# Performance work log

Measured on AMD Instinct MI355X. Metric: run time of the kernel, lower is better.

## Reference

```python
import math
import jax, jax.numpy as jnp
import numpy as np

NUM_HEADS = 16
D_MODEL = 1024
D_HEAD = 64
D_SEQ = 2048
NUM_LAYERS = 24
BATCH = 2


def setup_inputs() -> dict:
    key = jax.random.key(0)
    ks = jax.random.split(key, 10)
    s = math.sqrt(0.02)
    residual = jax.random.normal(ks[0], (BATCH, D_SEQ, D_MODEL), dtype=jnp.float32)
    W_Q = jax.random.normal(ks[1], (NUM_HEADS, D_MODEL, D_HEAD), dtype=jnp.float32) * s
    W_K = jax.random.normal(ks[2], (NUM_HEADS, D_MODEL, D_HEAD), dtype=jnp.float32) * s
    W_V = jax.random.normal(ks[3], (NUM_HEADS, D_MODEL, D_HEAD), dtype=jnp.float32) * s
    W_O = jax.random.normal(ks[4], (NUM_HEADS * D_HEAD, D_MODEL), dtype=jnp.float32) * s
    W_O = W_O / math.sqrt(NUM_LAYERS)
    b_Q = jax.random.normal(ks[5], (NUM_HEADS, D_HEAD), dtype=jnp.float32) * s
    b_K = jax.random.normal(ks[6], (NUM_HEADS, D_HEAD), dtype=jnp.float32) * s
    b_V = jax.random.normal(ks[7], (NUM_HEADS, D_HEAD), dtype=jnp.float32) * s
    b_O = jax.random.normal(ks[8], (D_MODEL,), dtype=jnp.float32) * s
    return dict(residual=residual, W_Q=W_Q, W_K=W_K, W_V=W_V, W_O=W_O,
                b_Q=b_Q, b_K=b_K, b_V=b_V, b_O=b_O)


def reference(residual, W_Q, W_K, W_V, W_O, b_Q, b_K, b_V, b_O):
    # residual: [b, s, m]; W_{Q,K,V}: [h, m, d]; b_{Q,K,V}: [h, d]
    Q = jnp.einsum('hmd,bsm->bshd', W_Q, residual) + b_Q
    K = jnp.einsum('hmd,bsm->bshd', W_K, residual) + b_K
    V = jnp.einsum('hmd,bsm->bshd', W_V, residual) + b_V
    # full causal score matrix [b, h, s_q, s_k], masked with -inf above diagonal
    QK = jnp.einsum('bqhd,bkhd->bhqk', Q, K)
    seq = residual.shape[1]
    causal = jnp.triu(jnp.ones((seq, seq), dtype=bool), k=1)  # True above diag
    QK_masked = jnp.where(causal, -jnp.inf, QK)
    soft = jax.nn.softmax(QK_masked / math.sqrt(D_HEAD), axis=-1)
    attn = jnp.einsum('bhqk,bkhd->bqhd', soft, V)  # [b, s, h, d]
    multi_head = attn.reshape(attn.shape[0], attn.shape[1], NUM_HEADS * D_HEAD)
    return jnp.einsum('em,bqe->bqm', W_O, multi_head) + b_O
```

## Files before the change

kernel.cpp:

```cpp
#include <hip/hip_runtime.h>
#include <stdint.h>

typedef unsigned short u16;
typedef unsigned long long u64;
typedef _Float16 f16;
typedef __attribute__((ext_vector_type(8))) _Float16 f16x8;
typedef __attribute__((ext_vector_type(4))) float f32x4;
typedef __attribute__((ext_vector_type(16))) float f32x16;
typedef __attribute__((ext_vector_type(4))) unsigned short u16x4;
typedef __attribute__((ext_vector_type(8))) unsigned short u16x8;

#define NHEADS 16
#define DMODEL 1024
#define DHEAD 64
#define SEQ 2048
#define NBATCH 2
#define MROWS (NBATCH * SEQ)
#define NQKV 3072
#define SCQ 0.18033688011112042f

__device__ __forceinline__ u16 f2h(float x) {
  union { f16 h; u16 u; } v;
  v.h = (f16)x;
  return v.u;
}

__device__ __forceinline__ unsigned pk2u(float x, float y) {
  typedef __fp16 fp16x2 __attribute__((ext_vector_type(2)));
  fp16x2 h = __builtin_amdgcn_cvt_pkrtz(x, y);
  union { fp16x2 h; unsigned u; } v; v.h = h;
  return v.u;
}

__device__ __forceinline__ f16x8 mkfrag(unsigned w0, unsigned w1, unsigned w2, unsigned w3) {
  union { unsigned u[4]; f16x8 f; } t;
  t.u[0] = w0; t.u[1] = w1; t.u[2] = w2; t.u[3] = w3;
  return t.f;
}

__device__ __forceinline__ f16x8 vfrag(const char* row, int sz, int F, int hib8) {
  union { u64 u[2]; f16x8 f; } t;
  t.u[0] = *(const u64*)(row + (((2 * F) ^ sz) << 4) + hib8);
  t.u[1] = *(const u64*)(row + (((2 * F + 1) ^ sz) << 4) + hib8);
  return t.f;
}

__device__ __forceinline__ void gload_lds16(const void* g, void* l) {
  __builtin_amdgcn_global_load_lds(
      (const __attribute__((address_space(1))) void*)g,
      (__attribute__((address_space(3))) void*)l, 16, 0, 0);
}

__global__ __launch_bounds__(256) void prep_kernel(
    const float* __restrict__ X,
    const float* __restrict__ WQ, const float* __restrict__ WK,
    const float* __restrict__ WV, const float* __restrict__ WO,
    u16* __restrict__ Xh, u16* __restrict__ Wqkv, u16* __restrict__ Wo) {
  __shared__ u16 lt[64][72];
  int blk = blockIdx.x;
  if (blk < 2048) {
    int i = blk * 256 + threadIdx.x;
    const f32x4* xv = (const f32x4*)(X + (size_t)i * 8);
    f32x4 a = xv[0], b = xv[1];
    u16x8 o;
    o[0] = f2h(a[0]); o[1] = f2h(a[1]); o[2] = f2h(a[2]); o[3] = f2h(a[3]);
    o[4] = f2h(b[0]); o[5] = f2h(b[1]); o[6] = f2h(b[2]); o[7] = f2h(b[3]);
    *(u16x8*)(Xh + (size_t)i * 8) = o;
  } else if (blk < 2816) {
    int bb = blk - 2048;
    int mt = bb & 15, hh = (bb >> 4) & 15, qkv = bb >> 8;
    const float* W = (qkv == 0) ? WQ : (qkv == 1) ? WK : WV;
    int m_in = threadIdx.x >> 2, dq = threadIdx.x & 3;
    const f32x4* sp4 = (const f32x4*)(W + (size_t)hh * (DMODEL * DHEAD) +
                                      (size_t)(mt * 64 + m_in) * DHEAD + dq * 16);
#pragma unroll
    for (int v4 = 0; v4 < 4; ++v4) {
      f32x4 a = sp4[v4];
#pragma unroll
      for (int j = 0; j < 4; ++j) lt[dq * 16 + v4 * 4 + j][m_in] = f2h(a[j]);
    }
    __syncthreads();
    int d_in = threadIdx.x >> 2, mq = threadIdx.x & 3;
    size_t orow = ((size_t)(qkv * 1024 + hh * 64 + d_in)) * DMODEL + mt * 64 + mq * 16;
    u16x8 o0, o1;
#pragma unroll
    for (int j = 0; j < 8; ++j) {
      o0[j] = lt[d_in][mq * 16 + j];
      o1[j] = lt[d_in][mq * 16 + 8 + j];
    }
    *(u16x8*)(Wqkv + orow) = o0;
    *(u16x8*)(Wqkv + orow + 8) = o1;
  } else {
    int bb = blk - 2816;
    int mt = bb & 15, et = bb >> 4;
    int e_in = threadIdx.x >> 2, mq = threadIdx.x & 3;
    const f32x4* sp4 = (const f32x4*)(WO + (size_t)(et * 64 + e_in) * DMODEL + mt * 64 + mq * 16);
#pragma unroll
    for (int v4 = 0; v4 < 4; ++v4) {
      f32x4 a = sp4[v4];
#pragma unroll
      for (int j = 0; j < 4; ++j) lt[mq * 16 + v4 * 4 + j][e_in] = f2h(a[j]);
    }
    __syncthreads();
    int m_in = threadIdx.x >> 2, eq = threadIdx.x & 3;
    size_t orow = (size_t)(mt * 64 + m_in) * DMODEL + et * 64 + eq * 16;
    u16x8 o0, o1;
#pragma unroll
    for (int j = 0; j < 8; ++j) {
      o0[j] = lt[m_in][eq * 16 + j];
      o1[j] = lt[m_in][eq * 16 + 8 + j];
    }
    *(u16x8*)(Wo + orow) = o0;
    *(u16x8*)(Wo + orow + 8) = o1;
  }
}

__global__ __launch_bounds__(256, 2) void gemm_qkv(
    const u16* __restrict__ A, const u16* __restrict__ Bt,
    const float* __restrict__ bq, const float* __restrict__ bk, const float* __restrict__ bv,
    u16* __restrict__ Qo, u16* __restrict__ Ko, u16* __restrict__ Vto) {
  __shared__ u16 lds[2][8192];
  const int tid = threadIdx.x;
  const int wid = tid >> 6, lane = tid & 63, lr = lane & 15, lg = lane >> 4;
  const int wr = wid >> 1, wc = wid & 1;
  const int brow = blockIdx.y * 128, bcol = blockIdx.x * 128;

  f32x4 acc[4][4];
#pragma unroll
  for (int i = 0; i < 4; ++i)
#pragma unroll
    for (int j = 0; j < 4; ++j) acc[i][j] = (f32x4){0.f, 0.f, 0.f, 0.f};

#define STAGE(buf, kt)                                                               \
  {                                                                                  \
    _Pragma("unroll") for (int i = 0; i < 2; ++i) {                                  \
      int idx = tid + i * 256;                                                       \
      gload_lds16(A + (size_t)(brow + (idx >> 2)) * 1024 + (kt) * 32 + (idx & 3) * 8,\
                  (char*)&lds[buf][0] + (wid * 64 + i * 256) * 16);                  \
    }                                                                                \
    _Pragma("unroll") for (int i = 0; i < 2; ++i) {                                  \
      int idx = tid + i * 256;                                                       \
      gload_lds16(Bt + (size_t)(bcol + (idx >> 2)) * 1024 + (kt) * 32 + (idx & 3) * 8,\
                  (char*)&lds[buf][4096] + (wid * 64 + i * 256) * 16);               \
    }                                                                                \
  }

  STAGE(0, 0);
  __syncthreads();
  int cur = 0;
  for (int kt = 0; kt < 32; ++kt) {
    if (kt + 1 < 32) STAGE(cur ^ 1, kt + 1);
    const u16* Ab = &lds[cur][0];
    const u16* Bb = &lds[cur][4096];
    f16x8 a[4], b[4];
#pragma unroll
    for (int ar = 0; ar < 4; ++ar)
      a[ar] = *(const f16x8*)(Ab + (wr * 64 + ar * 16 + lr) * 32 + lg * 8);
#pragma unroll
    for (int bc = 0; bc < 4; ++bc)
      b[bc] = *(const f16x8*)(Bb + (wc * 64 + bc * 16 + lr) * 32 + lg * 8);
#pragma unroll
    for (int ar = 0; ar < 4; ++ar)
#pragma unroll
      for (int bc = 0; bc < 4; ++bc)
        acc[ar][bc] = __builtin_amdgcn_mfma_f32_16x16x32_f16(a[ar], b[bc], acc[ar][bc], 0, 0, 0);
    __syncthreads();
    cur ^= 1;
  }

#pragma unroll
  for (int ar = 0; ar < 4; ++ar) {
    int row0 = brow + wr * 64 + ar * 16 + lg * 4;
    int bb = row0 >> 11, s0 = row0 & 2047;
#pragma unroll
    for (int bc = 0; bc < 4; ++bc) {
      int n = bcol + wc * 64 + bc * 16 + lr;
      int qkv = n >> 10, hd = n & 1023, h = hd >> 6, d = hd & 63;
      float bias = ((qkv == 0) ? bq : (qkv == 1) ? bk : bv)[hd];
      if (qkv < 2) {
        u16* dst = qkv ? Ko : Qo;
        float sc = qkv ? 1.f : SCQ;
        size_t base = ((size_t)(bb * NHEADS + h) * SEQ + s0) * DHEAD + d;
#pragma unroll
        for (int r = 0; r < 4; ++r)
          dst[base + (size_t)r * DHEAD] = f2h((acc[ar][bc][r] + bias) * sc);
      } else {
        u16x4 o;
        o[0] = f2h(acc[ar][bc][0] + bias);
        o[1] = f2h(acc[ar][bc][1] + bias);
        o[2] = f2h(acc[ar][bc][2] + bias);
        o[3] = f2h(acc[ar][bc][3] + bias);
        *(u16x4*)(Vto + ((size_t)(bb * NHEADS + h) * DHEAD + d) * SEQ + s0) = o;
      }
    }
  }
}

__global__ __launch_bounds__(256, 2) void gemm_out(
    const u16* __restrict__ A, const u16* __restrict__ Bt,
    const float* __restrict__ bo, float* __restrict__ Co) {
  __shared__ u16 lds[2][8192];
  const int tid = threadIdx.x;
  const int wid = tid >> 6, lane = tid & 63, lr = lane & 15, lg = lane >> 4;
  const int wr = wid >> 1, wc = wid & 1;
  const int brow = blockIdx.y * 128, bcol = blockIdx.x * 128;

  f32x4 acc[4][4];
#pragma unroll
  for (int i = 0; i < 4; ++i)
#pragma unroll
    for (int j = 0; j < 4; ++j) acc[i][j] = (f32x4){0.f, 0.f, 0.f, 0.f};

  STAGE(0, 0);
  __syncthreads();
  int cur = 0;
  for (int kt = 0; kt < 32; ++kt) {
    if (kt + 1 < 32) STAGE(cur ^ 1, kt + 1);
    const u16* Ab = &lds[cur][0];
    const u16* Bb = &lds[cur][4096];
    f16x8 a[4], b[4];
#pragma unroll
    for (int ar = 0; ar < 4; ++ar)
      a[ar] = *(const f16x8*)(Ab + (wr * 64 + ar * 16 + lr) * 32 + lg * 8);
#pragma unroll
    for (int bc = 0; bc < 4; ++bc)
      b[bc] = *(const f16x8*)(Bb + (wc * 64 + bc * 16 + lr) * 32 + lg * 8);
#pragma unroll
    for (int ar = 0; ar < 4; ++ar)
#pragma unroll
      for (int bc = 0; bc < 4; ++bc)
        acc[ar][bc] = __builtin_amdgcn_mfma_f32_16x16x32_f16(a[ar], b[bc], acc[ar][bc], 0, 0, 0);
    __syncthreads();
    cur ^= 1;
  }
#undef STAGE

#pragma unroll
  for (int ar = 0; ar < 4; ++ar) {
    int row0 = brow + wr * 64 + ar * 16 + lg * 4;
#pragma unroll
    for (int bc = 0; bc < 4; ++bc) {
      int n = bcol + wc * 64 + bc * 16 + lr;
      float bias = bo[n];
#pragma unroll
      for (int r = 0; r < 4; ++r)
        Co[(size_t)(row0 + r) * DMODEL + n] = acc[ar][bc][r] + bias;
    }
  }
}

__global__ __launch_bounds__(256, 2) void attn_kernel(
    const u16* __restrict__ Q, const u16* __restrict__ K,
    const u16* __restrict__ Vt, u16* __restrict__ MH) {
  __shared__ char sh8[32768];
  const int tid = threadIdx.x, wid = tid >> 6, lane = tid & 63;
  const int l31 = lane & 31, hi = lane >> 5;
  const int pairid = wid >> 1;
  const int qsub = wid & 1;
  const int bid = blockIdx.x;
  const int qidx = bid >> 5, bh = bid & 31;
  const int t = (qidx < 8) ? (31 - qidx) : (qidx < 16) ? (qidx - 8)
              : (qidx < 24) ? (39 - qidx) : (qidx - 16);
  const int h = bh & 15, b = bh >> 4;
  const u16* Qb = Q + (size_t)bh * (SEQ * DHEAD);
  const u16* Kb = K + (size_t)bh * (SEQ * DHEAD);
  const u16* Vb = Vt + (size_t)bh * (DHEAD * SEQ);

  const int sw0 = (l31 ^ (l31 >> 3)) & 7, kz0 = sw0 << 4;
  const int r32 = 32 + l31;
  const int sw1 = (r32 ^ (r32 >> 3)) & 7, kz1 = sw1 << 4;
  const int hib = hi * 16, hib8 = hi * 8;

#pragma unroll
  for (int i = 0; i < 2; ++i) {
    int idx = tid + i * 256, row = idx >> 3;
    int sseg = (idx & 7) ^ ((row ^ (row >> 3)) & 7);
    gload_lds16(Qb + (size_t)(t * 64 + row) * DHEAD + sseg * 8, sh8 + 16384 + idx * 16);
    gload_lds16(Kb + (size_t)row * DHEAD + sseg * 8, sh8 + idx * 16);
    if (t >= 1)
      gload_lds16(Kb + (size_t)(64 + row) * DHEAD + sseg * 8, sh8 + 8192 + idx * 16);
  }
  __syncthreads();

  f16x8 qf0, qf1, qf2, qf3;
  {
    int row = (qsub << 5) + l31;
    int swz = ((row ^ (row >> 3)) & 7) << 4;
    const char* qb = sh8 + 16384 + row * 128;
    qf0 = *(const f16x8*)(qb + ((hib + 0)  ^ swz));
    qf1 = *(const f16x8*)(qb + ((hib + 32) ^ swz));
    qf2 = *(const f16x8*)(qb + ((hib + 64) ^ swz));
    qf3 = *(const f16x8*)(qb + ((hib + 96) ^ swz));
  }
  __syncthreads();

#pragma unroll
  for (int i = 0; i < 2; ++i) {
    int idx = tid + i * 256, row = idx >> 3;
    int sseg = (idx & 7) ^ ((row ^ (row >> 3)) & 7);
    gload_lds16(Vb + (size_t)row * SEQ + sseg * 8, sh8 + 16384 + idx * 16);
    if (t >= 1)
      gload_lds16(Vb + (size_t)row * SEQ + 64 + sseg * 8, sh8 + 24576 + idx * 16);
  }

  f32x16 acc0, acc1;
#pragma unroll
  for (int z = 0; z < 16; ++z) { acc0[z] = 0.f; acc1[z] = 0.f; }
  float m = -1e30f, l = 0.f;
  const int qg = t * 64 + (qsub << 5) + l31;
  const int wall = (t >> 1) + 1;

  for (int si = 0; si < wall; ++si) {
    const int kt = 2 * si + pairid;
    const bool act = (kt <= t);
    f16x8 pa0, pa1, pa2, pa3;

    if (act) {
      const char* kbuf = sh8 + pairid * 8192;

      f32x16 s0, s1;
#pragma unroll
      for (int z = 0; z < 16; ++z) { s0[z] = 0.f; s1[z] = 0.f; }
      {
        const char* kb0 = kbuf + l31 * 128;
        const char* kb1 = kbuf + r32 * 128;
        f16x8 kf;
        __builtin_amdgcn_s_setprio(1);
        kf = *(const f16x8*)(kb0 + ((hib + 0)  ^ kz0)); s0 = __builtin_amdgcn_mfma_f32_32x32x16_f16(kf, qf0, s0, 0, 0, 0);
        kf = *(const f16x8*)(kb0 + ((hib + 32) ^ kz0)); s0 = __builtin_amdgcn_mfma_f32_32x32x16_f16(kf, qf1, s0, 0, 0, 0);
        kf = *(const f16x8*)(kb0 + ((hib + 64) ^ kz0)); s0 = __builtin_amdgcn_mfma_f32_32x32x16_f16(kf, qf2, s0, 0, 0, 0);
        kf = *(const f16x8*)(kb0 + ((hib + 96) ^ kz0)); s0 = __builtin_amdgcn_mfma_f32_32x32x16_f16(kf, qf3, s0, 0, 0, 0);
        kf = *(const f16x8*)(kb1 + ((hib + 0)  ^ kz1)); s1 = __builtin_amdgcn_mfma_f32_32x32x16_f16(kf, qf0, s1, 0, 0, 0);
        kf = *(const f16x8*)(kb1 + ((hib + 32) ^ kz1)); s1 = __builtin_amdgcn_mfma_f32_32x32x16_f16(kf, qf1, s1, 0, 0, 0);
        kf = *(const f16x8*)(kb1 + ((hib + 64) ^ kz1)); s1 = __builtin_amdgcn_mfma_f32_32x32x16_f16(kf, qf2, s1, 0, 0, 0);
        kf = *(const f16x8*)(kb1 + ((hib + 96) ^ kz1)); s1 = __builtin_amdgcn_mfma_f32_32x32x16_f16(kf, qf3, s1, 0, 0, 0);
        __builtin_amdgcn_s_setprio(0);
      }

      if (kt == t) {
#pragma unroll
        for (int rr = 0; rr < 16; ++rr) {
          int k0 = kt * 64 + (rr & 3) + 8 * (rr >> 2) + 4 * hi;
          if (k0 > qg) s0[rr] = -1e30f;
          if (k0 + 32 > qg) s1[rr] = -1e30f;
        }
      }

      float tm = s0[0];
#pragma unroll
      for (int rr = 1; rr < 16; ++rr) tm = fmaxf(tm, s0[rr]);
#pragma unroll
      for (int rr = 0; rr < 16; ++rr) tm = fmaxf(tm, s1[rr]);
      tm = fmaxf(tm, __shfl_xor(tm, 32));

      if (!__all(tm <= m + 8.f)) {
        float m2 = fmaxf(m, tm);
        float al = exp2f(m - m2);
        m = m2;
        l *= al;
#pragma unroll
        for (int rr = 0; rr < 16; ++rr) {
          int qp = (rr & 3) + 8 * (rr >> 2) + 4 * hi;
          float af = __shfl(al, qp);
          acc0[rr] *= af;
          acc1[rr] *= af;
        }
      }

      float rs = 0.f;
#pragma unroll
      for (int rr = 0; rr < 16; ++rr) { s0[rr] = exp2f(s0[rr] - m); rs += s0[rr]; }
#pragma unroll
      for (int rr = 0; rr < 16; ++rr) { s1[rr] = exp2f(s1[rr] - m); rs += s1[rr]; }
      rs += __shfl_xor(rs, 32);
      l += rs;

      pa0 = mkfrag(pk2u(s0[0],  s0[1]),  pk2u(s0[2],  s0[3]),
                   pk2u(s0[4],  s0[5]),  pk2u(s0[6],  s0[7]));
      pa1 = mkfrag(pk2u(s0[8],  s0[9]),  pk2u(s0[10], s0[11]),
                   pk2u(s0[12], s0[13]), pk2u(s0[14], s0[15]));
      pa2 = mkfrag(pk2u(s1[0],  s1[1]),  pk2u(s1[2],  s1[3]),
                   pk2u(s1[4],  s1[5]),  pk2u(s1[6],  s1[7]));
      pa3 = mkfrag(pk2u(s1[8],  s1[9]),  pk2u(s1[10], s1[11]),
                   pk2u(s1[12], s1[13]), pk2u(s1[14], s1[15]));
    }

    __syncthreads();

    const int e = 2 * si + 2;
    if (e <= t) {
#pragma unroll
      for (int i = 0; i < 2; ++i) {
        int idx = tid + i * 256, row = idx >> 3;
        int sseg = (idx & 7) ^ ((row ^ (row >> 3)) & 7);
        gload_lds16(Kb + (size_t)(e * 64 + row) * DHEAD + sseg * 8, sh8 + idx * 16);
        if (e + 1 <= t)
          gload_lds16(Kb + (size_t)((e + 1) * 64 + row) * DHEAD + sseg * 8,
                      sh8 + 8192 + idx * 16);
      }
    }

    if (act) {
      const char* vbuf = sh8 + 16384 + pairid * 8192;
      const char* vr0 = vbuf + l31 * 128;
      const char* vr1 = vbuf + r32 * 128;
      __builtin_amdgcn_s_setprio(1);
      acc0 = __builtin_amdgcn_mfma_f32_32x32x16_f16(pa0, vfrag(vr0, sw0, 0, hib8), acc0, 0, 0, 0);
      acc0 = __builtin_amdgcn_mfma_f32_32x32x16_f16(pa1, vfrag(vr0, sw0, 1, hib8), acc0, 0, 0, 0);
      acc0 = __builtin_amdgcn_mfma_f32_32x32x16_f16(pa2, vfrag(vr0, sw0, 2, hib8), acc0, 0, 0, 0);
      acc0 = __builtin_amdgcn_mfma_f32_32x32x16_f16(pa3, vfrag(vr0, sw0, 3, hib8), acc0, 0, 0, 0);
      acc1 = __builtin_amdgcn_mfma_f32_32x32x16_f16(pa0, vfrag(vr1, sw1, 0, hib8), acc1, 0, 0, 0);
      acc1 = __builtin_amdgcn_mfma_f32_32x32x16_f16(pa1, vfrag(vr1, sw1, 1, hib8), acc1, 0, 0, 0);
      acc1 = __builtin_amdgcn_mfma_f32_32x32x16_f16(pa2, vfrag(vr1, sw1, 2, hib8), acc1, 0, 0, 0);
      acc1 = __builtin_amdgcn_mfma_f32_32x32x16_f16(pa3, vfrag(vr1, sw1, 3, hib8), acc1, 0, 0, 0);
      __builtin_amdgcn_s_setprio(0);
    }

    __syncthreads();

    if (e <= t) {
#pragma unroll
      for (int i = 0; i < 2; ++i) {
        int idx = tid + i * 256, row = idx >> 3;
        int sseg = (idx & 7) ^ ((row ^ (row >> 3)) & 7);
        gload_lds16(Vb + (size_t)row * SEQ + e * 64 + sseg * 8, sh8 + 16384 + idx * 16);
        if (e + 1 <= t)
          gload_lds16(Vb + (size_t)row * SEQ + (e + 1) * 64 + sseg * 8,
                      sh8 + 24576 + idx * 16);
      }
    }
  }

  {
    const int slot = (qsub << 6) | (hi << 5) | l31;
    float* z = (float*)(sh8 + (pairid ? 16384 : 0)) + slot * 18;
    z[0] = m; z[1] = l;
#pragma unroll
    for (int rr = 0; rr < 16; ++rr) z[2 + rr] = pairid ? acc0[rr] : acc1[rr];
    __syncthreads();
    const float* y = (const float*)(sh8 + (pairid ? 0 : 16384)) + slot * 18;
    float mb = y[0], lb = y[1];
    float mM = fmaxf(m, mb);
    float aw = exp2f(m - mM), bw = exp2f(mb - mM);
    float lM = l * aw + lb * bw;
    const int d = pairid ? (32 + l31) : l31;
#pragma unroll
    for (int rr = 0; rr < 16; ++rr) {
      int qp = (rr & 3) + 8 * (rr >> 2) + 4 * hi;
      float aF = __shfl(aw, qp), bF = __shfl(bw, qp), lF = __shfl(lM, qp);
      float own = pairid ? acc1[rr] : acc0[rr];
      float val = (own * aF + y[2 + rr] * bF) / lF;
      int q = t * 64 + (qsub << 5) + qp;
      MH[((size_t)(b * SEQ) + q) * DMODEL + h * DHEAD + d] = f2h(val);
    }
  }
}

extern "C" void kernel_launch(void* const* d_in, const int* in_sizes, int n_in,
                              void* d_out, int out_size, void* d_ws, size_t ws_size,
                              hipStream_t stream) {
  const float* residual = (const float*)d_in[0];
  const float* WQ = (const float*)d_in[1];
  const float* WK = (const float*)d_in[2];
  const float* WV = (const float*)d_in[3];
  const float* WO = (const float*)d_in[4];
  const float* bQ = (const float*)d_in[5];
  const float* bK = (const float*)d_in[6];
  const float* bV = (const float*)d_in[7];
  const float* bO = (const float*)d_in[8];
  float* out = (float*)d_out;

  char* w = (char*)d_ws;
  u16* Xh   = (u16*)(w);
  u16* Wqkv = (u16*)(w + ((size_t)8 << 20));
  u16* Wo   = (u16*)(w + ((size_t)14 << 20));
  u16* Qd   = (u16*)(w + ((size_t)16 << 20));
  u16* Kd   = (u16*)(w + ((size_t)24 << 20));
  u16* Vtd  = (u16*)(w + ((size_t)32 << 20));
  u16* MH   = (u16*)(w + ((size_t)40 << 20));

  prep_kernel<<<3072, 256, 0, stream>>>(residual, WQ, WK, WV, WO, Xh, Wqkv, Wo);

  gemm_qkv<<<dim3(NQKV / 128, MROWS / 128), 256, 0, stream>>>(
      Xh, Wqkv, bQ, bK, bV, Qd, Kd, Vtd);

  attn_kernel<<<1024, 256, 0, stream>>>(Qd, Kd, Vtd, MH);

  gemm_out<<<dim3(DMODEL / 128, MROWS / 128), 256, 0, stream>>>(MH, Wo, bO, out);
}
```

Baseline: 113.2 us.

## Restructure causal attention into 8-wave blocks pairing complementary query tiles

The attention kernel now launches 512 blocks of 512 threads, and each block processes two query tiles (t and 31-t) one after the other, so every block does the same amount of causal work. Within a block, four key/value tile groups are processed in parallel by wave pairs. The partial softmax states are then merged with a two-level tree through shared memory. The K and V tiles for four key tiles are loaded together into 64KB of LDS per step. This replaces the older double-buffered prefetch, so loads no longer overlap with compute. The change aims to fix load imbalance and raise parallelism, at the cost of exposed load latency and a larger shared-memory footprint, which may reduce occupancy.

```diff
diff --git a/kernel.cpp b/kernel.cpp
--- a/kernel.cpp
+++ b/kernel.cpp
@@ -249,18 +249,16 @@
   }
 }
 
-__global__ __launch_bounds__(256, 2) void attn_kernel(
+__global__ __launch_bounds__(512, 2) void attn_kernel(
     const u16* __restrict__ Q, const u16* __restrict__ K,
     const u16* __restrict__ Vt, u16* __restrict__ MH) {
-  __shared__ char sh8[32768];
+  __shared__ char sh8[65536];
   const int tid = threadIdx.x, wid = tid >> 6, lane = tid & 63;
   const int l31 = lane & 31, hi = lane >> 5;
-  const int pairid = wid >> 1;
+  const int kp = wid >> 1;
   const int qsub = wid & 1;
   const int bid = blockIdx.x;
-  const int qidx = bid >> 5, bh = bid & 31;
-  const int t = (qidx < 8) ? (31 - qidx) : (qidx < 16) ? (qidx - 8)
-              : (qidx < 24) ? (39 - qidx) : (qidx - 16);
+  const int p = bid >> 5, bh = bid & 31;
   const int h = bh & 15, b = bh >> 4;
   const u16* Qb = Q + (size_t)bh * (SEQ * DHEAD);
   const u16* Kb = K + (size_t)bh * (SEQ * DHEAD);
@@ -271,187 +269,181 @@
   const int sw1 = (r32 ^ (r32 >> 3)) & 7, kz1 = sw1 << 4;
   const int hib = hi * 16, hib8 = hi * 8;
 
-#pragma unroll
-  for (int i = 0; i < 2; ++i) {
-    int idx = tid + i * 256, row = idx >> 3;
-    int sseg = (idx & 7) ^ ((row ^ (row >> 3)) & 7);
-    gload_lds16(Qb + (size_t)(t * 64 + row) * DHEAD + sseg * 8, sh8 + 16384 + idx * 16);
-    gload_lds16(Kb + (size_t)row * DHEAD + sseg * 8, sh8 + idx * 16);
-    if (t >= 1)
-      gload_lds16(Kb + (size_t)(64 + row) * DHEAD + sseg * 8, sh8 + 8192 + idx * 16);
-  }
-  __syncthreads();
-
-  f16x8 qf0, qf1, qf2, qf3;
-  {
-    int row = (qsub << 5) + l31;
-    int swz = ((row ^ (row >> 3)) & 7) << 4;
-    const char* qb = sh8 + 16384 + row * 128;
-    qf0 = *(const f16x8*)(qb + ((hib + 0)  ^ swz));
-    qf1 = *(const f16x8*)(qb + ((hib + 32) ^ swz));
-    qf2 = *(const f16x8*)(qb + ((hib + 64) ^ swz));
-    qf3 = *(const f16x8*)(qb + ((hib + 96) ^ swz));
-  }
-  __syncthreads();
-
-#pragma unroll
-  for (int i = 0; i < 2; ++i) {
-    int idx = tid + i * 256, row = idx >> 3;
-    int sseg = (idx & 7) ^ ((row ^ (row >> 3)) & 7);
-    gload_lds16(Vb + (size_t)row * SEQ + sseg * 8, sh8 + 16384 + idx * 16);
-    if (t >= 1)
-      gload_lds16(Vb + (size_t)row * SEQ + 64 + sseg * 8, sh8 + 24576 + idx * 16);
-  }
-
-  f32x16 acc0, acc1;
-#pragma unroll
-  for (int z = 0; z < 16; ++z) { acc0[z] = 0.f; acc1[z] = 0.f; }
-  float m = -1e30f, l = 0.f;
-  const int qg = t * 64 + (qsub << 5) + l31;
-  const int wall = (t >> 1) + 1;
-
-  for (int si = 0; si < wall; ++si) {
-    const int kt = 2 * si + pairid;
-    const bool act = (kt <= t);
-    f16x8 pa0, pa1, pa2, pa3;
-
-    if (act) {
-      const char* kbuf = sh8 + pairid * 8192;
-
-      f32x16 s0, s1;
-#pragma unroll
-      for (int z = 0; z < 16; ++z) { s0[z] = 0.f; s1[z] = 0.f; }
-      {
-        const char* kb0 = kbuf + l31 * 128;
-        const char* kb1 = kbuf + r32 * 128;
-        f16x8 kf;
+  const int srow = tid >> 3;
+  const int sseg = (tid & 7) ^ ((srow ^ (srow >> 3)) & 7);
+
+#pragma unroll
+  for (int seg = 0; seg < 2; ++seg) {
+    const int t = seg ? p : (31 - p);
+
+    gload_lds16(Qb + (size_t)(t * 64 + srow) * DHEAD + sseg * 8, sh8 + tid * 16);
+    __syncthreads();
+    f16x8 qf0, qf1, qf2, qf3;
+    {
+      int row = (qsub << 5) + l31;
+      int swz = ((row ^ (row >> 3)) & 7) << 4;
+      const char* qb = sh8 + row * 128;
+      qf0 = *(const f16x8*)(qb + ((hib + 0)  ^ swz));
+      qf1 = *(const f16x8*)(qb + ((hib + 32) ^ swz));
+      qf2 = *(const f16x8*)(qb + ((hib + 64) ^ swz));
+      qf3 = *(const f16x8*)(qb + ((hib + 96) ^ swz));
+    }
+    __syncthreads();
+
+    f32x16 acc0, acc1;
+#pragma unroll
+    for (int z = 0; z < 16; ++z) { acc0[z] = 0.f; acc1[z] = 0.f; }
+    float m = -1e30f, l = 0.f;
+    const int qg = t * 64 + (qsub << 5) + l31;
+    const int wall = (t >> 2) + 1;
+
+    for (int si = 0; si < wall; ++si) {
+#pragma unroll
+      for (int j = 0; j < 4; ++j) {
+        int e = 4 * si + j;
+        if (e <= t) {
+          gload_lds16(Kb + (size_t)(e * 64 + srow) * DHEAD + sseg * 8,
+                      sh8 + j * 8192 + tid * 16);
+          gload_lds16(Vb + (size_t)srow * SEQ + e * 64 + sseg * 8,
+                      sh8 + 32768 + j * 8192 + tid * 16);
+        }
+      }
+      __syncthreads();
+
+      const int kt = 4 * si + kp;
+      if (kt <= t) {
+        const char* kbuf = sh8 + kp * 8192;
+
+        f32x16 s0, s1;
+#pragma unroll
+        for (int z = 0; z < 16; ++z) { s0[z] = 0.f; s1[z] = 0.f; }
+        {
+          const char* kb0 = kbuf + l31 * 128;
+          const char* kb1 = kbuf + r32 * 128;
+          f16x8 kf;
+          __builtin_amdgcn_s_setprio(1);
+          kf = *(const f16x8*)(kb0 + ((hib + 0)  ^ kz0)); s0 = __builtin_amdgcn_mfma_f32_32x32x16_f16(kf, qf0, s0, 0, 0, 0);
+          kf = *(const f16x8*)(kb0 + ((hib + 32) ^ kz0)); s0 = __builtin_amdgcn_mfma_f32_32x32x16_f16(kf, qf1, s0, 0, 0, 0);
+          kf = *(const f16x8*)(kb0 + ((hib + 64) ^ kz0)); s0 = __builtin_amdgcn_mfma_f32_32x32x16_f16(kf, qf2, s0, 0, 0, 0);
+          kf = *(const f16x8*)(kb0 + ((hib + 96) ^ kz0)); s0 = __builtin_amdgcn_mfma_f32_32x32x16_f16(kf, qf3, s0, 0, 0, 0);
+          kf = *(const f16x8*)(kb1 + ((hib + 0)  ^ kz1)); s1 = __builtin_amdgcn_mfma_f32_32x32x16_f16(kf, qf0, s1, 0, 0, 0);
+          kf = *(const f16x8*)(kb1 + ((hib + 32) ^ kz1)); s1 = __builtin_amdgcn_mfma_f32_32x32x16_f16(kf, qf1, s1, 0, 0, 0);
+          kf = *(const f16x8*)(kb1 + ((hib + 64) ^ kz1)); s1 = __builtin_amdgcn_mfma_f32_32x32x16_f16(kf, qf2, s1, 0, 0, 0);
+          kf = *(const f16x8*)(kb1 + ((hib + 96) ^ kz1)); s1 = __builtin_amdgcn_mfma_f32_32x32x16_f16(kf, qf3, s1, 0, 0, 0);
+          __builtin_amdgcn_s_setprio(0);
+        }
+
+        if (kt == t) {
+#pragma unroll
+          for (int rr = 0; rr < 16; ++rr) {
+            int k0 = kt * 64 + (rr & 3) + 8 * (rr >> 2) + 4 * hi;
+            if (k0 > qg) s0[rr] = -1e30f;
+            if (k0 + 32 > qg) s1[rr] = -1e30f;
+          }
+        }
+
+        float tm = s0[0];
+#pragma unroll
+        for (int rr = 1; rr < 16; ++rr) tm = fmaxf(tm, s0[rr]);
+#pragma unroll
+        for (int rr = 0; rr < 16; ++rr) tm = fmaxf(tm, s1[rr]);
+        tm = fmaxf(tm, __shfl_xor(tm, 32));
+
+        if (!__all(tm <= m + 8.f)) {
+          float m2 = fmaxf(m, tm);
+          float al = exp2f(m - m2);
+          m = m2;
+          l *= al;
+#pragma unroll
+          for (int rr = 0; rr < 16; ++rr) {
+            int qp = (rr & 3) + 8 * (rr >> 2) + 4 * hi;
+            float af = __shfl(al, qp);
+            acc0[rr] *= af;
+            acc1[rr] *= af;
+          }
+        }
+
+        float rs = 0.f;
+#pragma unroll
+        for (int rr = 0; rr < 16; ++rr) { s0[rr] = exp2f(s0[rr] - m); rs += s0[rr]; }
+#pragma unroll
+        for (int rr = 0; rr < 16; ++rr) { s1[rr] = exp2f(s1[rr] - m); rs += s1[rr]; }
+        rs += __shfl_xor(rs, 32);
+        l += rs;
+
+        f16x8 pa0 = mkfrag(pk2u(s0[0],  s0[1]),  pk2u(s0[2],  s0[3]),
+                           pk2u(s0[4],  s0[5]),  pk2u(s0[6],  s0[7]));
+        f16x8 pa1 = mkfrag(pk2u(s0[8],  s0[9]),  pk2u(s0[10], s0[11]),
+                           pk2u(s0[12], s0[13]), pk2u(s0[14], s0[15]));
+        f16x8 pa2 = mkfrag(pk2u(s1[0],  s1[1]),  pk2u(s1[2],  s1[3]),
+                           pk2u(s1[4],  s1[5]),  pk2u(s1[6],  s1[7]));
+        f16x8 pa3 = mkfrag(pk2u(s1[8],  s1[9]),  pk2u(s1[10], s1[11]),
+                           pk2u(s1[12], s1[13]), pk2u(s1[14], s1[15]));
+
+        const char* vbuf = sh8 + 32768 + kp * 8192;
+        const char* vr0 = vbuf + l31 * 128;
+        const char* vr1 = vbuf + r32 * 128;
         __builtin_amdgcn_s_setprio(1);
-        kf = *(const f16x8*)(kb0 + ((hib + 0)  ^ kz0)); s0 = __builtin_amdgcn_mfma_f32_32x32x16_f16(kf, qf0, s0, 0, 0, 0);
-        kf = *(const f16x8*)(kb0 + ((hib + 32) ^ kz0)); s0 = __builtin_amdgcn_mfma_f32_32x32x16_f16(kf, qf1, s0, 0, 0, 0);
-        kf = *(const f16x8*)(kb0 + ((hib + 64) ^ kz0)); s0 = __builtin_amdgcn_mfma_f32_32x32x16_f16(kf, qf2, s0, 0, 0, 0);
-        kf = *(const f16x8*)(kb0 + ((hib + 96) ^ kz0)); s0 = __builtin_amdgcn_mfma_f32_32x32x16_f16(kf, qf3, s0, 0, 0, 0);
-        kf = *(const f16x8*)(kb1 + ((hib + 0)  ^ kz1)); s1 = __builtin_amdgcn_mfma_f32_32x32x16_f16(kf, qf0, s1, 0, 0, 0);
-        kf = *(const f16x8*)(kb1 + ((hib + 32) ^ kz1)); s1 = __builtin_amdgcn_mfma_f32_32x32x16_f16(kf, qf1, s1, 0, 0, 0);
-        kf = *(const f16x8*)(kb1 + ((hib + 64) ^ kz1)); s1 = __builtin_amdgcn_mfma_f32_32x32x16_f16(kf, qf2, s1, 0, 0, 0);
-        kf = *(const f16x8*)(kb1 + ((hib + 96) ^ kz1)); s1 = __builtin_amdgcn_mfma_f32_32x32x16_f16(kf, qf3, s1, 0, 0, 0);
+        acc0 = __builtin_amdgcn_mfma_f32_32x32x16_f16(pa0, vfrag(vr0, sw0, 0, hib8), acc0, 0, 0, 0);
+        acc0 = __builtin_amdgcn_mfma_f32_32x32x16_f16(pa1, vfrag(vr0, sw0, 1, hib8), acc0, 0, 0, 0);
+        acc0 = __builtin_amdgcn_mfma_f32_32x32x16_f16(pa2, vfrag(vr0, sw0, 2, hib8), acc0, 0, 0, 0);
+        acc0 = __builtin_amdgcn_mfma_f32_32x32x16_f16(pa3, vfrag(vr0, sw0, 3, hib8), acc0, 0, 0, 0);
+        acc1 = __builtin_amdgcn_mfma_f32_32x32x16_f16(pa0, vfrag(vr1, sw1, 0, hib8), acc1, 0, 0, 0);
+        acc1 = __builtin_amdgcn_mfma_f32_32x32x16_f16(pa1, vfrag(vr1, sw1, 1, hib8), acc1, 0, 0, 0);
+        acc1 = __builtin_amdgcn_mfma_f32_32x32x16_f16(pa2, vfrag(vr1, sw1, 2, hib8), acc1, 0, 0, 0);
+        acc1 = __builtin_amdgcn_mfma_f32_32x32x16_f16(pa3, vfrag(vr1, sw1, 3, hib8), acc1, 0, 0, 0);
         __builtin_amdgcn_s_setprio(0);
       }
-
-      if (kt == t) {
-#pragma unroll
-        for (int rr = 0; rr < 16; ++rr) {
-          int k0 = kt * 64 + (rr & 3) + 8 * (rr >> 2) + 4 * hi;
-          if (k0 > qg) s0[rr] = -1e30f;
-          if (k0 + 32 > qg) s1[rr] = -1e30f;
-        }
-      }
-
-      float tm = s0[0];
-#pragma unroll
-      for (int rr = 1; rr < 16; ++rr) tm = fmaxf(tm, s0[rr]);
-#pragma unroll
-      for (int rr = 0; rr < 16; ++rr) tm = fmaxf(tm, s1[rr]);
-      tm = fmaxf(tm, __shfl_xor(tm, 32));
-
-      if (!__all(tm <= m + 8.f)) {
-        float m2 = fmaxf(m, tm);
-        float al = exp2f(m - m2);
-        m = m2;
-        l *= al;
+      __syncthreads();
+    }
+
+    {
+      float* z = (float*)sh8 + (size_t)(wid * 64 + lane) * 18;
+      const bool keep0 = !(kp & 1);
+
+      z[0] = m; z[1] = l;
+#pragma unroll
+      for (int rr = 0; rr < 16; ++rr) z[2 + rr] = keep0 ? acc1[rr] : acc0[rr];
+      __syncthreads();
+      {
+        const float* y = (const float*)sh8 + (size_t)((wid ^ 2) * 64 + lane) * 18;
+        float mb = y[0], lb = y[1];
+        float mM = fmaxf(m, mb);
+        float aw = exp2f(m - mM), bw = exp2f(mb - mM);
+        float lM = l * aw + lb * bw;
 #pragma unroll
         for (int rr = 0; rr < 16; ++rr) {
           int qp = (rr & 3) + 8 * (rr >> 2) + 4 * hi;
-          float af = __shfl(al, qp);
-          acc0[rr] *= af;
-          acc1[rr] *= af;
-        }
+          float aF = __shfl(aw, qp), bF = __shfl(bw, qp);
+          if (keep0) acc0[rr] = acc0[rr] * aF + y[2 + rr] * bF;
+          else       acc1[rr] = acc1[rr] * aF + y[2 + rr] * bF;
+        }
+        m = mM; l = lM;
       }
-
-      float rs = 0.f;
-#pragma unroll
-      for (int rr = 0; rr < 16; ++rr) { s0[rr] = exp2f(s0[rr] - m); rs += s0[rr]; }
-#pragma unroll
-      for (int rr = 0; rr < 16; ++rr) { s1[rr] = exp2f(s1[rr] - m); rs += s1[rr]; }
-      rs += __shfl_xor(rs, 32);
-      l += rs;
-
-      pa0 = mkfrag(pk2u(s0[0],  s0[1]),  pk2u(s0[2],  s0[3]),
-                   pk2u(s0[4],  s0[5]),  pk2u(s0[6],  s0[7]));
-      pa1 = mkfrag(pk2u(s0[8],  s0[9]),  pk2u(s0[10], s0[11]),
-                   pk2u(s0[12], s0[13]), pk2u(s0[14], s0[15]));
-      pa2 = mkfrag(pk2u(s1[0],  s1[1]),  pk2u(s1[2],  s1[3]),
-                   pk2u(s1[4],  s1[5]),  pk2u(s1[6],  s1[7]));
-      pa3 = mkfrag(pk2u(s1[8],  s1[9]),  pk2u(s1[10], s1[11]),
-                   pk2u(s1[12], s1[13]), pk2u(s1[14], s1[15]));
-    }
-
-    __syncthreads();
-
-    const int e = 2 * si + 2;
-    if (e <= t) {
-#pragma unroll
-      for (int i = 0; i < 2; ++i) {
-        int idx = tid + i * 256, row = idx >> 3;
-        int sseg = (idx & 7) ^ ((row ^ (row >> 3)) & 7);
-        gload_lds16(Kb + (size_t)(e * 64 + row) * DHEAD + sseg * 8, sh8 + idx * 16);
-        if (e + 1 <= t)
-          gload_lds16(Kb + (size_t)((e + 1) * 64 + row) * DHEAD + sseg * 8,
-                      sh8 + 8192 + idx * 16);
+      __syncthreads();
+
+      z[0] = m; z[1] = l;
+#pragma unroll
+      for (int rr = 0; rr < 16; ++rr) z[2 + rr] = keep0 ? acc0[rr] : acc1[rr];
+      __syncthreads();
+      if (kp < 2) {
+        const float* y = (const float*)sh8 + (size_t)((wid ^ 4) * 64 + lane) * 18;
+        float mb = y[0], lb = y[1];
+        float mM = fmaxf(m, mb);
+        float aw = exp2f(m - mM), bw = exp2f(mb - mM);
+        float lM = l * aw + lb * bw;
+        const int d = keep0 ? l31 : (32 + l31);
+#pragma unroll
+        for (int rr = 0; rr < 16; ++rr) {
+          int qp = (rr & 3) + 8 * (rr >> 2) + 4 * hi;
+          float aF = __shfl(aw, qp), bF = __shfl(bw, qp), lF = __shfl(lM, qp);
+          float own = keep0 ? acc0[rr] : acc1[rr];
+          float val = (own * aF + y[2 + rr] * bF) / lF;
+          int q = t * 64 + (qsub << 5) + qp;
+          MH[((size_t)(b * SEQ) + q) * DMODEL + h * DHEAD + d] = f2h(val);
+        }
       }
-    }
-
-    if (act) {
-      const char* vbuf = sh8 + 16384 + pairid * 8192;
-      const char* vr0 = vbuf + l31 * 128;
-      const char* vr1 = vbuf + r32 * 128;
-      __builtin_amdgcn_s_setprio(1);
-      acc0 = __builtin_amdgcn_mfma_f32_32x32x16_f16(pa0, vfrag(vr0, sw0, 0, hib8), acc0, 0, 0, 0);
-      acc0 = __builtin_amdgcn_mfma_f32_32x32x16_f16(pa1, vfrag(vr0, sw0, 1, hib8), acc0, 0, 0, 0);
-      acc0 = __builtin_amdgcn_mfma_f32_32x32x16_f16(pa2, vfrag(vr0, sw0, 2, hib8), acc0, 0, 0, 0);
-      acc0 = __builtin_amdgcn_mfma_f32_32x32x16_f16(pa3, vfrag(vr0, sw0, 3, hib8), acc0, 0, 0, 0);
-      acc1 = __builtin_amdgcn_mfma_f32_32x32x16_f16(pa0, vfrag(vr1, sw1, 0, hib8), acc1, 0, 0, 0);
-      acc1 = __builtin_amdgcn_mfma_f32_32x32x16_f16(pa1, vfrag(vr1, sw1, 1, hib8), acc1, 0, 0, 0);
-      acc1 = __builtin_amdgcn_mfma_f32_32x32x16_f16(pa2, vfrag(vr1, sw1, 2, hib8), acc1, 0, 0, 0);
-      acc1 = __builtin_amdgcn_mfma_f32_32x32x16_f16(pa3, vfrag(vr1, sw1, 3, hib8), acc1, 0, 0, 0);
-      __builtin_amdgcn_s_setprio(0);
-    }
-
-    __syncthreads();
-
-    if (e <= t) {
-#pragma unroll
-      for (int i = 0; i < 2; ++i) {
-        int idx = tid + i * 256, row = idx >> 3;
-        int sseg = (idx & 7) ^ ((row ^ (row >> 3)) & 7);
-        gload_lds16(Vb + (size_t)row * SEQ + e * 64 + sseg * 8, sh8 + 16384 + idx * 16);
-        if (e + 1 <= t)
-          gload_lds16(Vb + (size_t)row * SEQ + (e + 1) * 64 + sseg * 8,
-                      sh8 + 24576 + idx * 16);
-      }
-    }
-  }
-
-  {
-    const int slot = (qsub << 6) | (hi << 5) | l31;
-    float* z = (float*)(sh8 + (pairid ? 16384 : 0)) + slot * 18;
-    z[0] = m; z[1] = l;
-#pragma unroll
-    for (int rr = 0; rr < 16; ++rr) z[2 + rr] = pairid ? acc0[rr] : acc1[rr];
-    __syncthreads();
-    const float* y = (const float*)(sh8 + (pairid ? 0 : 16384)) + slot * 18;
-    float mb = y[0], lb = y[1];
-    float mM = fmaxf(m, mb);
-    float aw = exp2f(m - mM), bw = exp2f(mb - mM);
-    float lM = l * aw + lb * bw;
-    const int d = pairid ? (32 + l31) : l31;
-#pragma unroll
-    for (int rr = 0; rr < 16; ++rr) {
-      int qp = (rr & 3) + 8 * (rr >> 2) + 4 * hi;
-      float aF = __shfl(aw, qp), bF = __shfl(bw, qp), lF = __shfl(lM, qp);
-      float own = pairid ? acc1[rr] : acc0[rr];
-      float val = (own * aF + y[2 + rr] * bF) / lF;
-      int q = t * 64 + (qsub << 5) + qp;
-      MH[((size_t)(b * SEQ) + q) * DMODEL + h * DHEAD + d] = f2h(val);
+      __syncthreads();
     }
   }
 }
@@ -484,7 +476,7 @@
   gemm_qkv<<<dim3(NQKV / 128, MROWS / 128), 256, 0, stream>>>(
       Xh, Wqkv, bQ, bK, bV, Qd, Kd, Vtd);
 
-  attn_kernel<<<1024, 256, 0, stream>>>(Qd, Kd, Vtd, MH);
+  attn_kernel<<<512, 512, 0, stream>>>(Qd, Kd, Vtd, MH);
 
   gemm_out<<<dim3(DMODEL / 128, MROWS / 128), 256, 0, stream>>>(MH, Wo, bO, out);
 }
```

New measurement: 132.0 us. 1.17x slower.
